# Kernel optimization log

Measured on AMD Instinct MI355X. Metric: run time of the kernel, lower is better.

## Reference

```python
import jax, jax.numpy as jnp
import numpy as np

HEADS = 16

def _split_heads(t, h):
    # 'b y (h d) -> (b h) y d'
    b, y, hd = t.shape
    d = hd // h
    return t.reshape(b, y, h, d).transpose(0, 2, 1, 3).reshape(b * h, y, d)

def _merge_heads(t, b, h):
    # '(b h) y d -> b y (h d)'
    bh, y, d = t.shape
    return t.reshape(b, h, y, d).transpose(0, 2, 1, 3).reshape(b, y, h * d)

def setup_inputs() -> dict:
    key = jax.random.key(0)
    ks = jax.random.split(key, 5)
    B, S, D = 8, 4096, 1024
    scale = 1.0 / np.sqrt(D)
    x = jax.random.normal(ks[0], (B, S, D), dtype=jnp.float32)
    Wq = jax.random.normal(ks[1], (D, D), dtype=jnp.float32) * scale
    Wk = jax.random.normal(ks[2], (D, D), dtype=jnp.float32) * scale
    Wv = jax.random.normal(ks[3], (D, D), dtype=jnp.float32) * scale
    Wo = jax.random.normal(ks[4], (D, D), dtype=jnp.float32) * scale
    return {"x": x, "Wq": Wq, "Wk": Wk, "Wv": Wv, "Wo": Wo}

def reference(x, Wq, Wk, Wv, Wo):
    b = x.shape[0]
    h = HEADS
    # torch nn.Linear stores weight as (out, in): y = x @ W.T
    q = _split_heads(x @ Wq.T, h)  # (b*h, y, d)
    k = _split_heads(x @ Wk.T, h)
    v = _split_heads(x @ Wv.T, h)
    d = q.shape[-1]
    # NOTE: faithfully contracts over the sequence axis y -> (b*h, d, d) scores
    z = jnp.einsum('byq,byk->bkq', q, k) / jnp.sqrt(jnp.asarray(d, x.dtype))
    z = jax.nn.softmax(z, axis=-1)
    z = jnp.einsum('byz,bvy->bvz', z, v)  # (b*h, seq, d)
    z = _merge_heads(z, b, h)             # (b, seq, h*d)
    # output projection (dropout is identity in eval)
    return z @ Wo.T
```

## Files before the change

### kernel.cpp

```cpp
#include <hip/hip_runtime.h>
#include <hip/hip_fp16.h>

typedef _Float16 f16;
typedef _Float16 f16x8 __attribute__((ext_vector_type(8)));
typedef _Float16 f16x4 __attribute__((ext_vector_type(4)));
typedef float    f32x4 __attribute__((ext_vector_type(4)));

#define MFMA16(a, b, c) __builtin_amdgcn_mfma_f32_16x16x32_f16((a), (b), (c), 0, 0, 0)

#define BARR() __builtin_amdgcn_s_barrier()
#define VMW6() asm volatile("s_waitcnt vmcnt(6)" ::: "memory")
#define VMW4() asm volatile("s_waitcnt vmcnt(4)" ::: "memory")
#define VMW0() asm volatile("s_waitcnt vmcnt(0)" ::: "memory")

#define GLOAD16(P, L)                                                          \
  __builtin_amdgcn_global_load_lds(                                            \
      (const __attribute__((address_space(1))) unsigned int*)(P),              \
      (__attribute__((address_space(3))) unsigned int*)(L), 16, 0, 0)

__global__ __launch_bounds__(256) void cast_f32_to_f16(const float* __restrict__ src,
                                                       f16* __restrict__ dst, int n4) {
  int i = blockIdx.x * 256 + threadIdx.x;
  if (i >= n4) return;
  float4 v = reinterpret_cast<const float4*>(src)[i];
  f16x4 o = { (f16)v.x, (f16)v.y, (f16)v.z, (f16)v.w };
  reinterpret_cast<f16x4*>(dst)[i] = o;
}

__global__ __launch_bounds__(256) void cast_weights(const float* __restrict__ Wq,
                                                    const float* __restrict__ Wk,
                                                    const float* __restrict__ Wv,
                                                    const float* __restrict__ Wo,
                                                    f16* __restrict__ wqkvh,
                                                    f16* __restrict__ woh) {
  const int k = blockIdx.x >> 10;
  const int i = (blockIdx.x & 1023) * 256 + threadIdx.x;
  const float* src = (k == 0) ? Wq : (k == 1) ? Wk : (k == 2) ? Wv : Wo;
  f16* dst = (k == 3) ? woh : (wqkvh + k * 1048576);
  float4 v = reinterpret_cast<const float4*>(src)[i];
  f16x4 o = { (f16)v.x, (f16)v.y, (f16)v.z, (f16)v.w };
  reinterpret_cast<f16x4*>(dst)[i] = o;
}

template <typename OutT>
__global__ __launch_bounds__(512, 1) void gemm_bt_8ph(const f16* __restrict__ A,
                                                      const f16* __restrict__ B,
                                                      OutT* __restrict__ C,
                                                      int N, int nbx) {
  constexpr int K = 1024;
  __shared__ f16 lds[2][2][2][8192];

  const int tid = threadIdx.x;
  const int wid = tid >> 6, l = tid & 63;
  const int wr = wid >> 2, wc = wid & 3;

  const int nwg = gridDim.x;
  const int cpx = nwg >> 3;
  const int id = blockIdx.x;
  const int swz = (id & 7) * cpx + (id >> 3);
  const int bx = swz % nbx, by = swz / nbx;

  int r0s, c0s, r1s, c1s;
  {
    int rel = tid * 16;
    int sub = rel >> 10, q = rel & 1023;
    int inner = q ^ (((q >> 9) & 1) << 5);
    r0s = ((sub >> 1) << 4) + (inner >> 6);
    c0s = ((sub & 1) << 5) + ((inner & 63) >> 1);
    rel = (512 + tid) * 16;
    sub = rel >> 10; q = rel & 1023;
    inner = q ^ (((q >> 9) & 1) << 5);
    r1s = ((sub >> 1) << 4) + (inner >> 6);
    c1s = ((sub & 1) << 5) + ((inner & 63) >> 1);
  }
  const f16* gA0a = A + (size_t)(by * 256 + r0s) * K + c0s;
  const f16* gA0b = A + (size_t)(by * 256 + r1s) * K + c1s;
  const f16* gA1a = gA0a + 128 * K;
  const f16* gA1b = gA0b + 128 * K;
  const f16* gB0a = B + (size_t)(bx * 256 + r0s) * K + c0s;
  const f16* gB0b = B + (size_t)(bx * 256 + r1s) * K + c1s;
  const f16* gB1a = gB0a + 128 * K;
  const f16* gB1b = gB0b + 128 * K;

#define STAGE_P(G0, G1, EOFF, LB, MAT, H)                                      \
  { GLOAD16((G0) + (EOFF), &lds[LB][MAT][H][wid * 512]);                       \
    GLOAD16((G1) + (EOFF), &lds[LB][MAT][H][4096 + wid * 512]); }

  const int lane_rd = (((l & 15) << 6) + ((l >> 4) << 4)) ^ (((l >> 3) & 1) << 5);
  const char* rdA0 = (const char*)&lds[0][0][wr][0] + lane_rd;
  const char* rdA1 = (const char*)&lds[1][0][wr][0] + lane_rd;
  const char* rdB0 = (const char*)&lds[0][1][wc >> 1][0] + (wc & 1) * 8192 + lane_rd;
  const char* rdB1 = (const char*)&lds[1][1][wc >> 1][0] + (wc & 1) * 8192 + lane_rd;

  f16x8 af[4][2], bf0[2][2], bf1[2][2];
  f32x4 acc[8][4] = {};

#define READ_A_MH(RD, mh)                                                      \
  _Pragma("unroll") for (int mm = 0; mm < 4; ++mm)                             \
  _Pragma("unroll") for (int ks = 0; ks < 2; ++ks)                             \
    af[mm][ks] = *reinterpret_cast<const f16x8*>(                              \
        (RD) + (((((mh)*4 + mm) * 2) + ks) << 10));
#define READ_B_NH(DST, RD, nh)                                                 \
  _Pragma("unroll") for (int nn = 0; nn < 2; ++nn)                             \
  _Pragma("unroll") for (int ks = 0; ks < 2; ++ks)                             \
    DST[nn][ks] = *reinterpret_cast<const f16x8*>(                             \
        (RD) + (((((nh)*2 + nn) * 2) + ks) << 10));
#define CL2(BF, mh, nh)                                                        \
  __builtin_amdgcn_s_setprio(1);                                               \
  _Pragma("unroll") for (int mm = 0; mm < 4; ++mm)                             \
  _Pragma("unroll") for (int nn = 0; nn < 2; ++nn)                             \
  _Pragma("unroll") for (int ks = 0; ks < 2; ++ks)                             \
    acc[(mh)*4 + mm][(nh)*2 + nn] =                                            \
        MFMA16(af[mm][ks], BF[nn][ks], acc[(mh)*4 + mm][(nh)*2 + nn]);         \
  __builtin_amdgcn_s_setprio(0);

  STAGE_P(gB0a, gB0b, 0, 0, 1, 0);
  STAGE_P(gB1a, gB1b, 0, 0, 1, 1);
  STAGE_P(gA0a, gA0b, 0, 0, 0, 0);
  STAGE_P(gA1a, gA1b, 0, 0, 0, 1);
  STAGE_P(gB0a, gB0b, 64, 1, 1, 0);
  STAGE_P(gB1a, gB1b, 64, 1, 1, 1);
  STAGE_P(gA0a, gA0b, 64, 1, 0, 0);
  VMW6();
  BARR();

  for (int i = 0; i < 8; ++i) {
    const bool more = (i < 7);
    READ_A_MH(rdA0, 0); READ_B_NH(bf0, rdB0, 0);
    STAGE_P(gA1a, gA1b, 64, 1, 0, 1);
    BARR(); CL2(bf0, 0, 0); BARR();
    READ_B_NH(bf1, rdB0, 1);
    BARR(); CL2(bf1, 0, 1); BARR();
    READ_A_MH(rdA0, 1);
    if (more) STAGE_P(gB0a, gB0b, 128, 0, 1, 0);
    BARR(); CL2(bf1, 1, 1); BARR();
    if (more) STAGE_P(gB1a, gB1b, 128, 0, 1, 1);
    BARR(); CL2(bf0, 1, 0);
    if (more) { VMW4(); } else { VMW0(); }
    BARR();
    READ_A_MH(rdA1, 0); READ_B_NH(bf0, rdB1, 0);
    if (more) STAGE_P(gA0a, gA0b, 128, 0, 0, 0);
    BARR(); CL2(bf0, 0, 0); BARR();
    READ_B_NH(bf1, rdB1, 1);
    if (more) STAGE_P(gA1a, gA1b, 128, 0, 0, 1);
    BARR(); CL2(bf1, 0, 1); BARR();
    READ_A_MH(rdA1, 1);
    if (more) STAGE_P(gB0a, gB0b, 192, 1, 1, 0);
    BARR(); CL2(bf1, 1, 1); BARR();
    if (more) { STAGE_P(gB1a, gB1b, 192, 1, 1, 1); STAGE_P(gA0a, gA0b, 192, 1, 0, 0); }
    BARR(); CL2(bf0, 1, 0);
    if (more) VMW6();
    BARR();
    gA0a += 128; gA0b += 128; gA1a += 128; gA1b += 128;
    gB0a += 128; gB0b += 128; gB1a += 128; gB1b += 128;
  }

  const int rr = by * 256 + wr * 128 + ((l >> 4) << 2);
  const int cc = bx * 256 + wc * 64 + (l & 15);
#pragma unroll
  for (int m = 0; m < 8; ++m)
#pragma unroll
    for (int n = 0; n < 4; ++n)
#pragma unroll
      for (int j = 0; j < 4; ++j)
        C[(size_t)(rr + m * 16 + j) * N + cc + n * 16] = (OutT)acc[m][n][j];
#undef STAGE_P
#undef READ_A_MH
#undef READ_B_NH
#undef CL2
}

__global__ __launch_bounds__(256, 2) void scores_part(const f16* __restrict__ qkv,
                                                      f16* __restrict__ part) {
  const int seg = blockIdx.x;
  const int bh = blockIdx.y;
  const int b = bh >> 4, h = bh & 15;
  const f16* base = qkv + (size_t)b * 4096 * 3072 + h * 64;

  __shared__ f16 sQ[64 * 264];
  __shared__ f16 sK[64 * 264];

  const int tid = threadIdx.x;
  const int w = tid >> 6, l = tid & 63;

  const int tsel = w >> 1;
  const int g = ((w & 1) << 6) + l;
  const int r0 = g >> 1;
  const int ch = g & 1;
  const f16* src = base + tsel * 1024 + (size_t)(seg * 256 + r0) * 3072 + ch * 32;
  f16* dstL = (tsel ? sK : sQ) + (ch * 32) * 264 + r0;

#pragma unroll
  for (int rep = 0; rep < 4; ++rep) {
    const f16* s0 = src + (size_t)(rep * 64) * 3072;
    f16x8 v0 = *reinterpret_cast<const f16x8*>(s0);
    f16x8 v1 = *reinterpret_cast<const f16x8*>(s0 + 8);
    f16x8 v2 = *reinterpret_cast<const f16x8*>(s0 + 16);
    f16x8 v3 = *reinterpret_cast<const f16x8*>(s0 + 24);
    f16* d = dstL + rep * 64;
#pragma unroll
    for (int j = 0; j < 8; ++j) {
      d[j * 264] = v0[j];
      d[(8 + j) * 264] = v1[j];
      d[(16 + j) * 264] = v2[j];
      d[(24 + j) * 264] = v3[j];
    }
  }
  __syncthreads();

  f32x4 acc[4] = {};
#pragma unroll
  for (int ys = 0; ys < 8; ++ys) {
    f16x8 a = *reinterpret_cast<const f16x8*>(sK + (w * 16 + (l & 15)) * 264 + ys * 32 + ((l >> 4) << 3));
#pragma unroll
    for (int n = 0; n < 4; ++n) {
      f16x8 bq = *reinterpret_cast<const f16x8*>(sQ + (n * 16 + (l & 15)) * 264 + ys * 32 + ((l >> 4) << 3));
      acc[n] = MFMA16(a, bq, acc[n]);
    }
  }

  f16* dst = part + ((size_t)(bh * 16 + seg)) * 4096;
#pragma unroll
  for (int n = 0; n < 4; ++n)
#pragma unroll
    for (int j = 0; j < 4; ++j)
      dst[(w * 16 + ((l >> 4) << 2) + j) * 64 + n * 16 + (l & 15)] = (f16)(acc[n][j] * 0.125f);
}

__global__ __launch_bounds__(256) void scores_combine(const f16* __restrict__ part,
                                                      f16* __restrict__ zt) {
  const int bh = blockIdx.x;
  const int kd = threadIdx.x >> 2;
  const int qg = threadIdx.x & 3;
  const f16* p0 = part + (size_t)bh * 16 * 4096 + kd * 64 + qg * 16;
  float s[16];
#pragma unroll
  for (int j = 0; j < 16; ++j) s[j] = 0.f;
#pragma unroll 4
  for (int seg = 0; seg < 16; ++seg) {
    f16x8 a = *reinterpret_cast<const f16x8*>(p0 + seg * 4096);
    f16x8 c = *reinterpret_cast<const f16x8*>(p0 + seg * 4096 + 8);
#pragma unroll
    for (int j = 0; j < 8; ++j) { s[j] += (float)a[j]; s[8 + j] += (float)c[j]; }
  }
  float mx = s[0];
#pragma unroll
  for (int j = 1; j < 16; ++j) mx = fmaxf(mx, s[j]);
  mx = fmaxf(mx, __shfl_xor(mx, 1));
  mx = fmaxf(mx, __shfl_xor(mx, 2));
  float sum = 0.f;
#pragma unroll
  for (int j = 0; j < 16; ++j) { float e = __expf(s[j] - mx); s[j] = e; sum += e; }
  sum += __shfl_xor(sum, 1);
  sum += __shfl_xor(sum, 2);
  float inv = 1.f / sum;
  f16* dst = zt + (size_t)bh * 4096 + (qg * 16) * 64 + kd;
#pragma unroll
  for (int j = 0; j < 16; ++j) dst[j * 64] = (f16)(s[j] * inv);
}

__global__ __launch_bounds__(256, 2) void pv_merge(const f16* __restrict__ qkv,
                                                   const f16* __restrict__ zt,
                                                   f16* __restrict__ out2) {
  const int st = blockIdx.x;
  const int bh = blockIdx.y;
  const int b = bh >> 4, h = bh & 15;
  const f16* vg = qkv + (size_t)(b * 4096 + st * 128) * 3072 + 2048 + h * 64;

  __shared__ f16 sV[128 * 72];
  __shared__ f16 sZ[64 * 72];

  const int tid = threadIdx.x;
  const int w = tid >> 6, l = tid & 63;

#pragma unroll
  for (int p = 0; p < 4; ++p) {
    int idx = (p * 256 + tid) * 8;
    int row = idx >> 6, col = idx & 63;
    f16x8 v = *reinterpret_cast<const f16x8*>(vg + (size_t)row * 3072 + col);
    *reinterpret_cast<f16x8*>(sV + row * 72 + col) = v;
  }
#pragma unroll
  for (int p = 0; p < 2; ++p) {
    int idx = (p * 256 + tid) * 8;
    int row = idx >> 6, col = idx & 63;
    f16x8 v = *reinterpret_cast<const f16x8*>(zt + (size_t)bh * 4096 + idx);
    *reinterpret_cast<f16x8*>(sZ + row * 72 + col) = v;
  }
  __syncthreads();

  f32x4 acc[2][4] = {};
#pragma unroll
  for (int ks = 0; ks < 2; ++ks) {
    f16x8 av[2], bz[4];
#pragma unroll
    for (int m = 0; m < 2; ++m)
      av[m] = *reinterpret_cast<const f16x8*>(sV + (w * 32 + m * 16 + (l & 15)) * 72 + ks * 32 + ((l >> 4) << 3));
#pragma unroll
    for (int n = 0; n < 4; ++n)
      bz[n] = *reinterpret_cast<const f16x8*>(sZ + (n * 16 + (l & 15)) * 72 + ks * 32 + ((l >> 4) << 3));
#pragma unroll
    for (int m = 0; m < 2; ++m)
#pragma unroll
      for (int n = 0; n < 4; ++n)
        acc[m][n] = MFMA16(av[m], bz[n], acc[m][n]);
  }

#pragma unroll
  for (int m = 0; m < 2; ++m)
#pragma unroll
    for (int n = 0; n < 4; ++n)
#pragma unroll
      for (int j = 0; j < 4; ++j) {
        int s = st * 128 + w * 32 + m * 16 + ((l >> 4) << 2) + j;
        out2[(size_t)(b * 4096 + s) * 1024 + h * 64 + n * 16 + (l & 15)] = (f16)acc[m][n][j];
      }
}

extern "C" void kernel_launch(void* const* d_in, const int* in_sizes, int n_in,
                              void* d_out, int out_size, void* d_ws, size_t ws_size,
                              hipStream_t stream) {
  const float* x  = (const float*)d_in[0];
  const float* Wq = (const float*)d_in[1];
  const float* Wk = (const float*)d_in[2];
  const float* Wv = (const float*)d_in[3];
  const float* Wo = (const float*)d_in[4];
  float* out = (float*)d_out;

  f16* xh    = (f16*)d_ws;
  f16* qkvh  = xh + 33554432;
  f16* wqkvh = qkvh + 100663296;
  f16* woh   = wqkvh + 3145728;
  f16* zth   = woh + 1048576;
  f16* out2h = zth + 524288;
  f16* part  = (f16*)d_ws;

  cast_f32_to_f16<<<32768, 256, 0, stream>>>(x, xh, 33554432 / 4);
  cast_weights<<<4096, 256, 0, stream>>>(Wq, Wk, Wv, Wo, wqkvh, woh);

  gemm_bt_8ph<f16><<<128 * 12, 512, 0, stream>>>(xh, wqkvh, qkvh, 3072, 12);

  scores_part<<<dim3(16, 128), 256, 0, stream>>>(qkvh, part);
  scores_combine<<<128, 256, 0, stream>>>(part, zth);

  pv_merge<<<dim3(32, 128), 256, 0, stream>>>(qkvh, zth, out2h);

  gemm_bt_8ph<float><<<128 * 4, 512, 0, stream>>>(out2h, woh, out, 1024, 4);
}
```

Before: 384.7 us.

## Software-pipeline LDS fragment reads ahead of MFMA clusters in GEMM main loop

```diff
diff --git a/kernel.cpp b/kernel.cpp
--- a/kernel.cpp
+++ b/kernel.cpp
@@ -10,7 +10,7 @@
 
 #define BARR() __builtin_amdgcn_s_barrier()
 #define VMW6() asm volatile("s_waitcnt vmcnt(6)" ::: "memory")
-#define VMW4() asm volatile("s_waitcnt vmcnt(4)" ::: "memory")
+#define VMW2() asm volatile("s_waitcnt vmcnt(2)" ::: "memory")
 #define VMW0() asm volatile("s_waitcnt vmcnt(0)" ::: "memory")
 
 #define GLOAD16(P, L)                                                          \
@@ -123,33 +123,49 @@
   STAGE_P(gA0a, gA0b, 64, 1, 0, 0);
   VMW6();
   BARR();
+  READ_A_MH(rdA0, 0);
+  READ_B_NH(bf0, rdB0, 0);
 
   for (int i = 0; i < 8; ++i) {
     const bool more = (i < 7);
-    READ_A_MH(rdA0, 0); READ_B_NH(bf0, rdB0, 0);
     STAGE_P(gA1a, gA1b, 64, 1, 0, 1);
-    BARR(); CL2(bf0, 0, 0); BARR();
+    BARR();
+    CL2(bf0, 0, 0);
     READ_B_NH(bf1, rdB0, 1);
-    BARR(); CL2(bf1, 0, 1); BARR();
+    BARR();
+    BARR();
+    CL2(bf1, 0, 1);
     READ_A_MH(rdA0, 1);
+    BARR();
     if (more) STAGE_P(gB0a, gB0b, 128, 0, 1, 0);
-    BARR(); CL2(bf1, 1, 1); BARR();
-    if (more) STAGE_P(gB1a, gB1b, 128, 0, 1, 1);
-    BARR(); CL2(bf0, 1, 0);
-    if (more) { VMW4(); } else { VMW0(); }
-    BARR();
-    READ_A_MH(rdA1, 0); READ_B_NH(bf0, rdB1, 0);
-    if (more) STAGE_P(gA0a, gA0b, 128, 0, 0, 0);
-    BARR(); CL2(bf0, 0, 0); BARR();
+    BARR();
+    CL2(bf1, 1, 1);
+    if (more) { VMW2(); } else { VMW0(); }
+    BARR();
+    if (more) { STAGE_P(gB1a, gB1b, 128, 0, 1, 1); STAGE_P(gA0a, gA0b, 128, 0, 0, 0); }
+    BARR();
+    CL2(bf0, 1, 0);
+    READ_A_MH(rdA1, 0);
+    READ_B_NH(bf0, rdB1, 0);
+    BARR();
+    if (more) STAGE_P(gA1a, gA1b, 128, 0, 0, 1);
+    BARR();
+    CL2(bf0, 0, 0);
     READ_B_NH(bf1, rdB1, 1);
-    if (more) STAGE_P(gA1a, gA1b, 128, 0, 0, 1);
-    BARR(); CL2(bf1, 0, 1); BARR();
+    BARR();
+    BARR();
+    CL2(bf1, 0, 1);
     READ_A_MH(rdA1, 1);
+    BARR();
     if (more) STAGE_P(gB0a, gB0b, 192, 1, 1, 0);
-    BARR(); CL2(bf1, 1, 1); BARR();
+    BARR();
+    CL2(bf1, 1, 1);
+    if (more) VMW2();
+    BARR();
     if (more) { STAGE_P(gB1a, gB1b, 192, 1, 1, 1); STAGE_P(gA0a, gA0b, 192, 1, 0, 0); }
-    BARR(); CL2(bf0, 1, 0);
-    if (more) VMW6();
+    BARR();
+    CL2(bf0, 1, 0);
+    if (more) { READ_A_MH(rdA0, 0); READ_B_NH(bf0, rdB0, 0); }
     BARR();
     gA0a += 128; gA0b += 128; gA1a += 128; gA1b += 128;
     gB0a += 128; gB0b += 128; gB1a += 128; gB1b += 128;
```

Result: no change. 384.9 us (median of 2 runs) (+0.1%).
